# Performance work log

Hardware: AMD Instinct MI355X
Metric: run time of the kernel (lower is better)

## Reference

```python
import jax, jax.numpy as jnp
import numpy as np


def _mlp(x, W0, b0, W1, b1, W2, b2, W3, b3):
    # 4-layer MLP, ReLU between layers, no final activation
    h = jax.nn.relu(x @ W0 + b0)
    h = jax.nn.relu(h @ W1 + b1)
    h = jax.nn.relu(h @ W2 + b2)
    return h @ W3 + b3


def setup_inputs() -> dict:
    key = jax.random.key(0)
    ks = jax.random.split(key, 8)
    B, t, p, f = 4, 12, 32, 64          # num_graphs, timesteps, n_patches, nhid
    n = 10000                            # nodes per graph
    E = 200000                           # subgraph-node membership entries
    in_dim = f * t + t                   # 780
    horizon = 12
    scale = 0.02
    return {
        "mixer_x": jax.random.normal(ks[0], (B, t, p, f), jnp.float32),
        "features": jax.random.normal(ks[1], (B * n, t), jnp.float32),
        "subgraphs_batch": jax.random.randint(ks[2], (E,), 0, p * B),
        "subgraphs_nodes_mapper": jax.random.randint(ks[3], (E,), 0, n * B),
        "W0": jax.random.normal(ks[4], (in_dim, in_dim), jnp.float32) * scale,
        "b0": jnp.zeros((in_dim,), jnp.float32),
        "W1": jax.random.normal(ks[5], (in_dim, in_dim), jnp.float32) * scale,
        "b1": jnp.zeros((in_dim,), jnp.float32),
        "W2": jax.random.normal(ks[6], (in_dim, in_dim), jnp.float32) * scale,
        "b2": jnp.zeros((in_dim,), jnp.float32),
        "W3": jax.random.normal(ks[7], (in_dim, horizon), jnp.float32) * scale,
        "b3": jnp.zeros((horizon,), jnp.float32),
    }


def reference(mixer_x, features, subgraphs_batch, subgraphs_nodes_mapper,
              W0, b0, W1, b1, W2, b2, W3, b3):
    B, t, p, f = mixer_x.shape
    n_seg = features.shape[0]                      # n * B segments
    n = n_seg // B
    # passthrough: '(B n) t -> B n t'
    passthrough = features.reshape(B, n, t)
    # mixer_x: 'B t p f -> (p B) t f'
    flat = jnp.transpose(mixer_x, (2, 0, 1, 3)).reshape(p * B, t, f)
    # gather by subgraph index, then scatter-mean over node mapper
    gathered = flat[subgraphs_batch]               # (E, t, f)
    sums = jax.ops.segment_sum(gathered, subgraphs_nodes_mapper, num_segments=n_seg)
    counts = jax.ops.segment_sum(jnp.ones((gathered.shape[0],), gathered.dtype),
                                 subgraphs_nodes_mapper, num_segments=n_seg)
    nodes = sums / jnp.maximum(counts, 1.0)[:, None, None]   # (n*B, t, f)
    # '(n B) t f -> B n (t f)'
    nodes = jnp.transpose(nodes.reshape(n, B, t, f), (1, 0, 2, 3)).reshape(B, n, t * f)
    mlp_in = jnp.concatenate([passthrough, nodes], axis=-1)  # (B, n, t + t*f)
    mlp_out = _mlp(mlp_in, W0, b0, W1, b1, W2, b2, W3, b3)   # (B, n, horizon)
    # 'B n h -> (B n) h'
    return mlp_out.reshape(B * n, -1)
```

## Files before the change

kernel.cpp:

```cpp
#include <hip/hip_runtime.h>

#define BG    4
#define TT    12
#define NN    10000
#define EN    200000
#define NSEG  40000
#define NROWS 40000
#define MPAD  40064
#define KD    832
#define KA0   160
#define NPW   896
#define NT    7
#define KW3   896

typedef __attribute__((ext_vector_type(8))) short bf8_t;
typedef __attribute__((ext_vector_type(4))) float f4_t;

__device__ __forceinline__ unsigned short f2bf(float x) {
  unsigned int u = __float_as_uint(x);
  u += 0x7fffu + ((u >> 16) & 1u);
  return (unsigned short)(u >> 16);
}

#define GLDS16(src, dst) __builtin_amdgcn_global_load_lds( \
    (const __attribute__((address_space(1))) void*)(src),  \
    (__attribute__((address_space(3))) void*)(dst), 16, 0, 0)

#define LKW0 asm volatile("s_waitcnt lgkmcnt(0)" ::: "memory")
#define VMW0 asm volatile("s_waitcnt vmcnt(0)" ::: "memory")
#define VMW4 asm volatile("s_waitcnt vmcnt(4)" ::: "memory")
#define VMW8 asm volatile("s_waitcnt vmcnt(8)" ::: "memory")
#define SBAR0 __builtin_amdgcn_sched_barrier(0)

__global__ void k_init(int* __restrict__ counts, float* __restrict__ Cff,
                       float* __restrict__ out3, const float* __restrict__ b3) {
  int i = blockIdx.x * 256 + threadIdx.x;
  if (i < NSEG) counts[i] = 0;
  if (i < MPAD * 128) Cff[i] = 0.f;
  if (i < NROWS * 12) out3[i] = b3[i % 12];
}

__global__ void k_count(const int* __restrict__ mapper, int* __restrict__ counts) {
  int e = blockIdx.x * 256 + threadIdx.x;
  if (e < EN) atomicAdd(&counts[mapper[e]], 1);
}

__global__ void k_scatterCf(const int* __restrict__ mapper, const int* __restrict__ batch,
                            float* __restrict__ Cff) {
  int e = blockIdx.x * 256 + threadIdx.x;
  if (e < EN) {
    const int s = mapper[e];
    const int r = (s % BG) * NN + s / BG;
    atomicAdd(&Cff[(size_t)r * 128 + batch[e]], 1.0f);
  }
}

__global__ void k_buildA(const float* __restrict__ features, const int* __restrict__ counts,
                         const float* __restrict__ Cff, unsigned short* __restrict__ A) {
  int idx = blockIdx.x * 256 + threadIdx.x;
  if (idx >= MPAD * KA0) return;
  const int r = idx / KA0, c = idx - r * KA0;
  float v = 0.f;
  if (r < NROWS) {
    if (c < 12) {
      v = features[(size_t)r * TT + c];
    } else if (c < 140) {
      const int s = (r % NN) * BG + (r / NN);
      const int cnt = counts[s];
      const float inv = 1.f / (float)(cnt > 0 ? cnt : 1);
      v = Cff[(size_t)r * 128 + (c - 12)] * inv;
    }
  }
  A[idx] = f2bf(v);
}

__global__ void k_prep(const float* __restrict__ W0, const float* __restrict__ fW0,
                       const float* __restrict__ W1, const float* __restrict__ W2,
                       const float* __restrict__ W3,
                       const float* __restrict__ b0, const float* __restrict__ b1,
                       const float* __restrict__ b2,
                       unsigned short* __restrict__ Wt1, unsigned short* __restrict__ Wt2,
                       unsigned short* __restrict__ Wt3,
                       float* __restrict__ bp0, float* __restrict__ bp1,
                       float* __restrict__ bp2, unsigned short* __restrict__ WTB) {
  constexpr int S1 = NPW * KD;
  constexpr int S3 = 16 * KW3;
  constexpr int SB = 3 * NPW;
  constexpr int S5 = NPW * KA0;
  int idx = blockIdx.x * 256 + threadIdx.x;
  if (idx < 2 * S1) {
    const int which = idx / S1, rem = idx - which * S1;
    const int n = rem / KD, k = rem - n * KD;
    const float* W = which ? W2 : W1;
    float v = (n < 780 && k < 780) ? W[(size_t)k * 780 + n] : 0.f;
    (which ? Wt2 : Wt1)[rem] = f2bf(v);
    return;
  }
  idx -= 2 * S1;
  if (idx < S3) {
    const int n = idx / KW3, k = idx - n * KW3;
    float v = (n < 12 && k < 780) ? W3[(size_t)k * 12 + n] : 0.f;
    Wt3[idx] = f2bf(v);
    return;
  }
  idx -= S3;
  if (idx < SB) {
    const int which = idx / NPW, c = idx - which * NPW;
    const float* src = which == 0 ? b0 : (which == 1 ? b1 : b2);
    float* dst = which == 0 ? bp0 : (which == 1 ? bp1 : bp2);
    dst[c] = (c < 780) ? src[c] : 0.f;
    return;
  }
  idx -= SB;
  if (idx < S5) {
    const int n = idx / KA0, k = idx - n * KA0;
    float v = 0.f;
    if (n < 780) {
      if (k < 12) v = W0[(size_t)k * 780 + n];
      else if (k < 140) v = fW0[(size_t)(k - 12) * KD + n];
    }
    WTB[idx] = f2bf(v);
  }
}

__global__ __launch_bounds__(256) void k_flatW0(const float* __restrict__ mixer,
                                                const float* __restrict__ W0,
                                                float* __restrict__ fW0) {
  __shared__ float sA[8][768];
  __shared__ float sRed[4][64][9];
  const int tid = threadIdx.x;
  const int c0 = blockIdx.x * 64, j0 = blockIdx.y * 8;
  for (int i = tid; i < 8 * 768; i += 256) {
    int jj = i / 768;
    int k = i - jj * 768;
    int j = j0 + jj;
    int tt = k >> 6, ff = k & 63;
    sA[jj][k] = mixer[(((j & 3) * TT + tt) * 32 + (j >> 2)) * 64 + ff];
  }
  __syncthreads();
  const int cc = tid & 63, ks = tid >> 6;
  const int c = c0 + cc;
  float acc[8] = {};
  if (c < 780) {
    const float* wp = W0 + (size_t)(12 + ks * 192) * 780 + c;
    #pragma unroll 4
    for (int k = ks * 192; k < ks * 192 + 192; ++k) {
      const float w = *wp; wp += 780;
      #pragma unroll
      for (int jj = 0; jj < 8; ++jj) acc[jj] = fmaf(sA[jj][k], w, acc[jj]);
    }
  }
  #pragma unroll
  for (int jj = 0; jj < 8; ++jj) sRed[ks][cc][jj] = acc[jj];
  __syncthreads();
  for (int o = tid; o < 512; o += 256) {
    const int oc = o & 63, jj = o >> 6;
    const int wc = c0 + oc;
    if (wc < KD) {
      float s = sRed[0][oc][jj] + sRed[1][oc][jj] + sRed[2][oc][jj] + sRed[3][oc][jj];
      fW0[(size_t)(j0 + jj) * KD + wc] = s;
    }
  }
}

template<int KA, bool FUSE>
__global__ __launch_bounds__(256) void gemm_relu(
    const unsigned short* __restrict__ A, const unsigned short* __restrict__ WT,
    const float* __restrict__ bias, unsigned short* __restrict__ C,
    const unsigned short* __restrict__ W3t, float* __restrict__ out3) {
  constexpr int BK   = 32;
  constexpr int SEGR = BK / 8;
  constexpr int MASK = SEGR - 1;
  constexpr int NISS = (128 * SEGR) / 256;
  constexpr int NKT  = KA / BK;
  constexpr int BUFB = 128 * BK * 2;
  __shared__ char smem[3 * 2 * BUFB];
  const int tid = threadIdx.x, lane = tid & 63, wid = tid >> 6;
  const int wm = wid >> 1, wn = wid & 1;

  const int nwg = gridDim.x;
  const int q = nwg >> 3, r8 = nwg & 7;
  const int xcd = blockIdx.x & 7, bidx = blockIdx.x >> 3;
  const int linear = (xcd < r8 ? xcd * (q + 1) : r8 * (q + 1) + (xcd - r8) * q) + bidx;
  const int rowtile = linear / NT, ntile = linear - rowtile * NT;

  const int row0 = rowtile * 128, n0 = ntile * 128;
  const char* gA = (const char*)A + (size_t)row0 * (KA * 2);
  const char* gB = (const char*)WT + (size_t)n0 * (KA * 2);
  const int frow = lane & 15;

  int offA[4], offB[4];
  {
    const int c16r = lane >> 4;
    #pragma unroll
    for (int i = 0; i < 4; ++i) {
      const int ra = wm * 64 + i * 16 + frow;
      const int rb = wn * 64 + i * 16 + frow;
      offA[i] = ra * (BK * 2) + ((c16r ^ (ra & MASK)) * 16);
      offB[i] = rb * (BK * 2) + ((c16r ^ (rb & MASK)) * 16);
    }
  }

  auto bufA = [&](int b) { return smem + b * 2 * BUFB; };
  auto bufB = [&](int b) { return smem + b * 2 * BUFB + BUFB; };

  auto stage = [&](int b, int kt) {
    const int kb = kt * (BK * 2);
    #pragma unroll
    for (int L = 0; L < NISS; ++L) {
      const int seg = L * 256 + wid * 64 + lane;
      const int row = seg / SEGR, c16 = seg & MASK;
      const int c16s = c16 ^ (row & MASK);
      const size_t go = (size_t)row * (KA * 2) + kb + c16s * 16;
      GLDS16(gA + go, bufA(b) + seg * 16);
      GLDS16(gB + go, bufB(b) + seg * 16);
    }
  };

  f4_t acc[4][4] = {};

  stage(0, 0);
  stage(1, 1);
  stage(2, 2);
  VMW8;
  __builtin_amdgcn_s_barrier();

  #pragma unroll
  for (int t = 0; t < NKT; ++t) {
    const int cur = t % 3;
    bf8_t af[4], bfv[4];
    #pragma unroll
    for (int i = 0; i < 4; ++i) {
      af[i]  = *(const bf8_t*)(bufA(cur) + offA[i]);
      bfv[i] = *(const bf8_t*)(bufB(cur) + offB[i]);
    }
    if (t < NKT - 1) {
      LKW0;
      __builtin_amdgcn_s_barrier();
      SBAR0;
      if (t + 3 < NKT) stage(cur, t + 3);
    } else {
      LKW0;
      SBAR0;
    }
    __builtin_amdgcn_s_setprio(1);
    #pragma unroll
    for (int mi = 0; mi < 4; ++mi)
      #pragma unroll
      for (int ni = 0; ni < 4; ++ni)
        acc[mi][ni] = __builtin_amdgcn_mfma_f32_16x16x32_bf16(bfv[ni], af[mi], acc[mi][ni], 0, 0, 0);
    __builtin_amdgcn_s_setprio(0);
    if (t < NKT - 1) {
      if (t + 3 < NKT)      { VMW8; }
      else if (t + 2 < NKT) { VMW4; }
      else                  { VMW0; }
      __builtin_amdgcn_s_barrier();
    }
  }

  const int cq = (lane >> 4) * 4;
  if constexpr (!FUSE) {
    #pragma unroll
    for (int mi = 0; mi < 4; ++mi) {
      const int r = row0 + wm * 64 + mi * 16 + frow;
      unsigned short* crow = C + (size_t)r * KD;
      #pragma unroll
      for (int ni = 0; ni < 4; ++ni) {
        const int c = n0 + wn * 64 + ni * 16 + cq;
        if (c < KD) {
          f4_t v = acc[mi][ni];
          const f4_t bb = *(const f4_t*)(bias + c);
          float v0 = fmaxf(v[0] + bb[0], 0.f);
          float v1 = fmaxf(v[1] + bb[1], 0.f);
          float v2 = fmaxf(v[2] + bb[2], 0.f);
          float v3 = fmaxf(v[3] + bb[3], 0.f);
          uint2 pk;
          pk.x = (unsigned int)f2bf(v0) | ((unsigned int)f2bf(v1) << 16);
          pk.y = (unsigned int)f2bf(v2) | ((unsigned int)f2bf(v3) << 16);
          *(uint2*)(crow + c) = pk;
        }
      }
    }
  } else {
    unsigned short* sT = (unsigned short*)smem;
    __syncthreads();
    #pragma unroll
    for (int mi = 0; mi < 4; ++mi) {
      const int lr = wm * 64 + mi * 16 + frow;
      #pragma unroll
      for (int ni = 0; ni < 4; ++ni) {
        const int lc = wn * 64 + ni * 16 + cq;
        f4_t v = acc[mi][ni];
        const f4_t bb = *(const f4_t*)(bias + (n0 + lc));
        float v0 = fmaxf(v[0] + bb[0], 0.f);
        float v1 = fmaxf(v[1] + bb[1], 0.f);
        float v2 = fmaxf(v[2] + bb[2], 0.f);
        float v3 = fmaxf(v[3] + bb[3], 0.f);
        uint2 pk;
        pk.x = (unsigned int)f2bf(v0) | ((unsigned int)f2bf(v1) << 16);
        pk.y = (unsigned int)f2bf(v2) | ((unsigned int)f2bf(v3) << 16);
        const int bo = (lr * 256 + lc * 2) ^ ((lr & 7) << 4);
        *(uint2*)((char*)sT + bo) = pk;
      }
    }
    __syncthreads();
    const int fk = (lane >> 4) * 8;
    f4_t acc2[2] = {};
    #pragma unroll
    for (int kk2 = 0; kk2 < 4; ++kk2) {
      const bf8_t bw = *(const bf8_t*)(W3t + (size_t)frow * KW3 + n0 + kk2 * 32 + fk);
      #pragma unroll
      for (int mi2 = 0; mi2 < 2; ++mi2) {
        const int lr2 = wid * 32 + mi2 * 16 + frow;
        const int bo = (lr2 * 256 + (kk2 * 32 + fk) * 2) ^ ((lr2 & 7) << 4);
        const bf8_t av = *(const bf8_t*)((char*)sT + bo);
        acc2[mi2] = __builtin_amdgcn_mfma_f32_16x16x32_bf16(bw, av, acc2[mi2], 0, 0, 0);
      }
    }
    #pragma unroll
    for (int mi2 = 0; mi2 < 2; ++mi2) {
      const int r2 = row0 + wid * 32 + mi2 * 16 + frow;
      if (r2 < NROWS && cq < 12) {
        float* orow = out3 + (size_t)r2 * 12 + cq;
        atomicAdd(&orow[0], acc2[mi2][0]);
        atomicAdd(&orow[1], acc2[mi2][1]);
        atomicAdd(&orow[2], acc2[mi2][2]);
        atomicAdd(&orow[3], acc2[mi2][3]);
      }
    }
  }
}

extern "C" void kernel_launch(void* const* d_in, const int* in_sizes, int n_in,
                              void* d_out, int out_size, void* d_ws, size_t ws_size,
                              hipStream_t stream) {
  const float* mixer    = (const float*)d_in[0];
  const float* features = (const float*)d_in[1];
  const int*   sg_batch = (const int*)d_in[2];
  const int*   sg_map   = (const int*)d_in[3];
  const float* W0 = (const float*)d_in[4];  const float* b0 = (const float*)d_in[5];
  const float* W1 = (const float*)d_in[6];  const float* b1 = (const float*)d_in[7];
  const float* W2 = (const float*)d_in[8];  const float* b2 = (const float*)d_in[9];
  const float* W3 = (const float*)d_in[10]; const float* b3 = (const float*)d_in[11];
  float* out = (float*)d_out;

  char* wsp = (char*)d_ws;
  auto alloc = [&](size_t bytes) { char* p = wsp; wsp += (bytes + 255) & ~(size_t)255; return p; };
  unsigned short* h0  = (unsigned short*)alloc((size_t)MPAD * KD * 2);
  unsigned short* h1  = (unsigned short*)alloc((size_t)MPAD * KD * 2);
  unsigned short* Wt1 = (unsigned short*)alloc((size_t)NPW * KD * 2);
  unsigned short* Wt2 = (unsigned short*)alloc((size_t)NPW * KD * 2);
  unsigned short* Wt3 = (unsigned short*)alloc((size_t)16 * KW3 * 2);
  unsigned short* WTB = (unsigned short*)alloc((size_t)NPW * KA0 * 2);
  float* bp0   = (float*)alloc(NPW * 4);
  float* bp1   = (float*)alloc(NPW * 4);
  float* bp2   = (float*)alloc(NPW * 4);
  float* fW0   = (float*)alloc((size_t)128 * KD * 4);
  int* counts  = (int*)alloc(NSEG * 4);
  float* Cff = (float*)h1;
  unsigned short* Abuf = (unsigned short*)((char*)h1 + ((size_t)MPAD * 128 * 4 + 255 & ~(size_t)255));

  k_init<<<(MPAD * 128 + 255) / 256, 256, 0, stream>>>(counts, Cff, out, b3);
  k_count<<<(EN + 255) / 256, 256, 0, stream>>>(sg_map, counts);
  k_scatterCf<<<(EN + 255) / 256, 256, 0, stream>>>(sg_map, sg_batch, Cff);

  k_flatW0<<<dim3(13, 16), 256, 0, stream>>>(mixer, W0, fW0);
  {
    const int total = 2 * (NPW * KD) + 16 * KW3 + 3 * NPW + NPW * KA0;
    k_prep<<<(total + 255) / 256, 256, 0, stream>>>(W0, fW0, W1, W2, W3, b0, b1, b2,
                                                    Wt1, Wt2, Wt3, bp0, bp1, bp2, WTB);
  }

  k_buildA<<<(MPAD * KA0 + 255) / 256, 256, 0, stream>>>(features, counts, Cff, Abuf);

  gemm_relu<KA0, false><<<(MPAD / 128) * NT, 256, 0, stream>>>(Abuf, WTB, bp0, h0, nullptr, nullptr);

  gemm_relu<KD, false><<<(MPAD / 128) * NT, 256, 0, stream>>>(h0, Wt1, bp1, h1, nullptr, nullptr);

  gemm_relu<KD, true><<<(MPAD / 128) * NT, 256, 0, stream>>>(h1, Wt2, bp2, nullptr, Wt3, out);
}
```

Baseline: 341.9 us.

## Fuse edge scatter kernels, use memsets, coalesce weight prep reads, retune LDS swizzle

Merges the count and Cff scatter kernels into one edge pass and replaces the zero-init kernel with hipMemsetAsync, shrinking the Cff clear to NROWS rows. Reorders the prep index mapping so reads of W1/W2/W0 are coalesced along n, with transposed writes instead. Changes the LDS XOR swizzle to key on row>>1, aiming to reduce bank conflicts on the fragment loads. The swizzle change has to stay consistent between the staging writes and the fragment reads, and both sides are updated.

```diff
diff --git a/kernel.cpp b/kernel.cpp
--- a/kernel.cpp
+++ b/kernel.cpp
@@ -32,24 +32,17 @@
 #define VMW8 asm volatile("s_waitcnt vmcnt(8)" ::: "memory")
 #define SBAR0 __builtin_amdgcn_sched_barrier(0)
 
-__global__ void k_init(int* __restrict__ counts, float* __restrict__ Cff,
-                       float* __restrict__ out3, const float* __restrict__ b3) {
+__global__ void k_outinit(float* __restrict__ out3, const float* __restrict__ b3) {
   int i = blockIdx.x * 256 + threadIdx.x;
-  if (i < NSEG) counts[i] = 0;
-  if (i < MPAD * 128) Cff[i] = 0.f;
   if (i < NROWS * 12) out3[i] = b3[i % 12];
 }
 
-__global__ void k_count(const int* __restrict__ mapper, int* __restrict__ counts) {
-  int e = blockIdx.x * 256 + threadIdx.x;
-  if (e < EN) atomicAdd(&counts[mapper[e]], 1);
-}
-
-__global__ void k_scatterCf(const int* __restrict__ mapper, const int* __restrict__ batch,
-                            float* __restrict__ Cff) {
+__global__ void k_edges(const int* __restrict__ mapper, const int* __restrict__ batch,
+                        int* __restrict__ counts, float* __restrict__ Cff) {
   int e = blockIdx.x * 256 + threadIdx.x;
   if (e < EN) {
     const int s = mapper[e];
+    atomicAdd(&counts[s], 1);
     const int r = (s % BG) * NN + s / BG;
     atomicAdd(&Cff[(size_t)r * 128 + batch[e]], 1.0f);
   }
@@ -90,10 +83,10 @@
   int idx = blockIdx.x * 256 + threadIdx.x;
   if (idx < 2 * S1) {
     const int which = idx / S1, rem = idx - which * S1;
-    const int n = rem / KD, k = rem - n * KD;
+    const int k = rem / NPW, n = rem - k * NPW;
     const float* W = which ? W2 : W1;
     float v = (n < 780 && k < 780) ? W[(size_t)k * 780 + n] : 0.f;
-    (which ? Wt2 : Wt1)[rem] = f2bf(v);
+    (which ? Wt2 : Wt1)[(size_t)n * KD + k] = f2bf(v);
     return;
   }
   idx -= 2 * S1;
@@ -113,13 +106,13 @@
   }
   idx -= SB;
   if (idx < S5) {
-    const int n = idx / KA0, k = idx - n * KA0;
+    const int k = idx / NPW, n = idx - k * NPW;
     float v = 0.f;
     if (n < 780) {
       if (k < 12) v = W0[(size_t)k * 780 + n];
       else if (k < 140) v = fW0[(size_t)(k - 12) * KD + n];
     }
-    WTB[idx] = f2bf(v);
+    WTB[(size_t)n * KA0 + k] = f2bf(v);
   }
 }
 
@@ -196,8 +189,8 @@
     for (int i = 0; i < 4; ++i) {
       const int ra = wm * 64 + i * 16 + frow;
       const int rb = wn * 64 + i * 16 + frow;
-      offA[i] = ra * (BK * 2) + ((c16r ^ (ra & MASK)) * 16);
-      offB[i] = rb * (BK * 2) + ((c16r ^ (rb & MASK)) * 16);
+      offA[i] = ra * (BK * 2) + ((c16r ^ ((ra >> 1) & MASK)) * 16);
+      offB[i] = rb * (BK * 2) + ((c16r ^ ((rb >> 1) & MASK)) * 16);
     }
   }
 
@@ -210,7 +203,7 @@
     for (int L = 0; L < NISS; ++L) {
       const int seg = L * 256 + wid * 64 + lane;
       const int row = seg / SEGR, c16 = seg & MASK;
-      const int c16s = c16 ^ (row & MASK);
+      const int c16s = c16 ^ ((row >> 1) & MASK);
       const size_t go = (size_t)row * (KA * 2) + kb + c16s * 16;
       GLDS16(gA + go, bufA(b) + seg * 16);
       GLDS16(gB + go, bufB(b) + seg * 16);
@@ -358,11 +351,13 @@
   float* fW0   = (float*)alloc((size_t)128 * KD * 4);
   int* counts  = (int*)alloc(NSEG * 4);
   float* Cff = (float*)h1;
-  unsigned short* Abuf = (unsigned short*)((char*)h1 + ((size_t)MPAD * 128 * 4 + 255 & ~(size_t)255));
-
-  k_init<<<(MPAD * 128 + 255) / 256, 256, 0, stream>>>(counts, Cff, out, b3);
-  k_count<<<(EN + 255) / 256, 256, 0, stream>>>(sg_map, counts);
-  k_scatterCf<<<(EN + 255) / 256, 256, 0, stream>>>(sg_map, sg_batch, Cff);
+  unsigned short* Abuf = (unsigned short*)((char*)h1 + (((size_t)NROWS * 128 * 4 + 255) & ~(size_t)255));
+
+  hipMemsetAsync(counts, 0, NSEG * 4, stream);
+  hipMemsetAsync(Cff, 0, (size_t)NROWS * 128 * 4, stream);
+  k_outinit<<<(NROWS * 12 + 255) / 256, 256, 0, stream>>>(out, b3);
+
+  k_edges<<<(EN + 255) / 256, 256, 0, stream>>>(sg_map, sg_batch, counts, Cff);
 
   k_flatW0<<<dim3(13, 16), 256, 0, stream>>>(mixer, W0, fW0);
   {
```

Result: no change. 342.7 us (+0.2%).
